# Kernel tuning notes

Measured on AMD Instinct MI355X. Metric: run time of the kernel, lower is better.

Reference implementation:

```python
import jax, jax.numpy as jnp
import numpy as np
from jax import lax

B, T, I, H = 64, 512, 512, 512


def setup_inputs() -> dict:
    key = jax.random.key(0)
    ks = jax.random.split(key, 9)
    s_in = 1.0 / np.sqrt(I)
    s_h = 1.0 / np.sqrt(H)
    return {
        "x": jax.random.normal(ks[0], (B, T, I), dtype=jnp.float32),
        "h0_f": jnp.zeros((B, H), dtype=jnp.float32),
        "h0_b": jnp.zeros((B, H), dtype=jnp.float32),
        # cell_f params (torch Linear: y = x @ W.T + b)
        "Wxf_w": jax.random.uniform(ks[1], (H, I), jnp.float32, -s_in, s_in),
        "Wxf_b": jax.random.uniform(ks[2], (H,), jnp.float32, -s_in, s_in),
        "Whf_w": jax.random.uniform(ks[3], (H, H), jnp.float32, -s_h, s_h),
        # cell_b params
        "Wxb_w": jax.random.uniform(ks[4], (H, I), jnp.float32, -s_in, s_in),
        "Wxb_b": jax.random.uniform(ks[5], (H,), jnp.float32, -s_in, s_in),
        "Whb_w": jax.random.uniform(ks[6], (H, H), jnp.float32, -s_h, s_h),
    }


def _run_dir(x_tbi, h0, Wx_w, Wx_b, Wh_w, reverse):
    # Precompute input projections as one big GEMM (same math as per-step Linear)
    xproj = jnp.einsum("tbi,hi->tbh", x_tbi, Wx_w) + Wx_b  # (T,B,H)

    def step(h, xp):
        h = jnp.tanh(xp + h @ Wh_w.T)
        return h, h

    hT, hs = lax.scan(step, h0, xproj, reverse=reverse)
    return hT, hs  # hs in natural time order even when reverse=True


def reference(x, h0_f, h0_b, Wxf_w, Wxf_b, Whf_w, Wxb_w, Wxb_b, Whb_w):
    x_tbi = jnp.transpose(x, (1, 0, 2))  # (T,B,I)
    hT_f, hs_f = _run_dir(x_tbi, h0_f, Wxf_w, Wxf_b, Whf_w, reverse=False)
    hT_b, hs_b = _run_dir(x_tbi, h0_b, Wxb_w, Wxb_b, Whb_w, reverse=True)
    y = jnp.concatenate([hs_f, hs_b], axis=-1)  # (T,B,2H)
    y = jnp.transpose(y, (1, 0, 2))  # (B,T,2H)
    return y, hT_f, hT_b
```

## Files before the change

### kernel.cpp

```cpp
#include <hip/hip_runtime.h>

#define T_LEN 512
#define B_SZ  64
#define I_SZ  512
#define H_SZ  512

using half8   = __attribute__((ext_vector_type(8))) _Float16;
using half4   = __attribute__((ext_vector_type(4))) _Float16;
using float4v = __attribute__((ext_vector_type(4))) float;

__device__ __forceinline__ float fast_tanh(float x) {
    float e = __expf(2.0f * x);
    return 1.0f - 2.0f * __builtin_amdgcn_rcpf(e + 1.0f);
}

__global__ __launch_bounds__(256) void xproj_kernel(
    const float* __restrict__ x,
    const float* __restrict__ Wf, const float* __restrict__ bf,
    const float* __restrict__ Wb, const float* __restrict__ bb,
    _Float16* __restrict__ xp)
{
    __shared__ _Float16 Ash[64][72];
    __shared__ _Float16 Bsh[64][72];

    const int bid = blockIdx.x;
    const int dir = bid & 1;
    const int nt  = (bid >> 1) & 7;
    const int t   = bid >> 4;
    const float* __restrict__ W    = dir ? Wb : Wf;
    const float* __restrict__ bias = dir ? bb : bf;
    const int n0 = nt * 64;

    const int tid  = threadIdx.x;
    const int row  = tid >> 2;
    const int part = tid & 3;
    const int wv   = tid >> 6;
    const int lane = tid & 63;
    const int lm   = lane & 15;
    const int lq   = lane >> 4;

    float4v acc[4] = {{0,0,0,0},{0,0,0,0},{0,0,0,0},{0,0,0,0}};

    const float* ap = x + ((size_t)row * T_LEN + t) * I_SZ + part * 16;
    const float* bp = W + ((size_t)(n0 + row)) * I_SZ + part * 16;

    for (int k0 = 0; k0 < I_SZ; k0 += 64) {
        float areg[16], breg[16];
        #pragma unroll
        for (int i = 0; i < 16; i++) { areg[i] = ap[k0 + i]; breg[i] = bp[k0 + i]; }
        __syncthreads();
        #pragma unroll
        for (int i = 0; i < 16; i++) {
            Ash[row][part*16 + i] = (_Float16)areg[i];
            Bsh[row][part*16 + i] = (_Float16)breg[i];
        }
        __syncthreads();
        #pragma unroll
        for (int ks = 0; ks < 2; ks++) {
            half8 afr = *(const half8*)&Ash[16*wv + lm][ks*32 + lq*8];
            #pragma unroll
            for (int ns = 0; ns < 4; ns++) {
                half8 bfr = *(const half8*)&Bsh[ns*16 + lm][ks*32 + lq*8];
                acc[ns] = __builtin_amdgcn_mfma_f32_16x16x32_f16(afr, bfr, acc[ns], 0, 0, 0);
            }
        }
    }

    #pragma unroll
    for (int ns = 0; ns < 4; ns++) {
        const int n = n0 + ns*16 + lm;
        const float bv = bias[n];
        #pragma unroll
        for (int j = 0; j < 4; j++) {
            const int b = 16*wv + lq*4 + j;
            xp[(((size_t)dir*T_LEN + t)*B_SZ + b)*H_SZ + n] = (_Float16)(acc[ns][j] + bv);
        }
    }
}

__global__ __launch_bounds__(512, 2) void rnn_kernel(
    const _Float16* __restrict__ xp,
    const float* __restrict__ Whf, const float* __restrict__ Whb,
    const float* __restrict__ h0f, const float* __restrict__ h0b,
    float* __restrict__ out)
{
    const int blk  = blockIdx.x;
    const int dir  = blk >> 2;
    const int b0   = (blk & 3) * 16;
    const int tid  = threadIdx.x;
    const int wv   = tid >> 6;
    const int lane = tid & 63;
    const int lq   = lane >> 4;
    const int lm   = lane & 15;

    const float* __restrict__ Wh = dir ? Whb : Whf;
    const float* __restrict__ h0 = dir ? h0b : h0f;

    __shared__ _Float16 hl[8192];
    __shared__ _Float16 wl[8][16][64][8];

    half8 bw[4][12];
    {
        const float* wr0 = Wh + ((size_t)(wv*64 + lm*4)) * H_SZ + lq*8;
        #pragma unroll
        for (int nt = 0; nt < 4; nt++) {
            const float* wr = wr0 + (size_t)nt * H_SZ;
            #pragma unroll
            for (int kt = 0; kt < 16; kt++) {
                float4v lo = *(const float4v*)(wr + kt*32);
                float4v hi = *(const float4v*)(wr + kt*32 + 4);
                half8 v;
                #pragma unroll
                for (int e = 0; e < 4; e++) { v[e] = (_Float16)lo[e]; v[e+4] = (_Float16)hi[e]; }
                if (kt < 12) bw[nt][kt] = v;
                else *(half8*)&wl[wv][nt*4 + (kt - 12)][lane][0] = v;
            }
        }
    }

    #pragma unroll
    for (int r = 0; r < 2; r++) {
        const int gi  = r*512 + tid;
        const int khi = gi >> 4;
        const int b   = gi & 15;
        const float* p = h0 + (size_t)(b0 + b)*H_SZ + khi*8;
        half8 v;
        #pragma unroll
        for (int e = 0; e < 8; e++) v[e] = (_Float16)p[e];
        *(half8*)&hl[(khi*16 + (b ^ (khi & 15))) * 8] = v;
    }
    __syncthreads();

    const _Float16* wlp = &wl[wv][0][lane][0];

    const int ts = dir ? -1 : 1;
    const int t0 = dir ? (T_LEN - 1) : 0;
    const _Float16* xpt = xp + (((size_t)dir*T_LEN + t0)*B_SZ + (b0 + lq*4))*H_SZ
                             + wv*64 + lm*4;
    const ptrdiff_t xstep = (ptrdiff_t)ts * (B_SZ * H_SZ);
    float* yb = out + ((size_t)(b0 + lq*4)*T_LEN + t0)*1024 + dir*512 + wv*64 + lm*4;
    const ptrdiff_t ystep = (ptrdiff_t)ts * 1024;

    const int khiw = wv*8 + (lm >> 1);
    const int gofs = (lm & 1) * 4;

    half4 xq[4];
    #pragma unroll
    for (int j = 0; j < 4; j++) xq[j] = *(const half4*)(xpt + j*H_SZ);

    #pragma unroll 1
    for (int s = 0; s < T_LEN; s++) {
        float4v acc[4];
        #pragma unroll
        for (int nt = 0; nt < 4; nt++)
            #pragma unroll
            for (int j = 0; j < 4; j++)
                acc[nt][j] = (float)xq[j][nt];

        if (s + 1 < T_LEN) {
            xpt += xstep;
            #pragma unroll
            for (int j = 0; j < 4; j++) xq[j] = *(const half4*)(xpt + j*H_SZ);
        }

        #pragma unroll
        for (int g = 0; g < 3; g++) {
            half8 af[4];
            #pragma unroll
            for (int i = 0; i < 4; i++) {
                const int c = (g*4 + i)*4 + lq;
                af[i] = *(const half8*)&hl[(c*16 + (lm ^ (c & 15))) * 8];
            }
            #pragma unroll
            for (int i = 0; i < 4; i++)
                #pragma unroll
                for (int nt = 0; nt < 4; nt++)
                    acc[nt] = __builtin_amdgcn_mfma_f32_16x16x32_f16(af[i], bw[nt][g*4 + i], acc[nt], 0, 0, 0);
        }
        {
            half8 af[4];
            #pragma unroll
            for (int i = 0; i < 4; i++) {
                const int c = (12 + i)*4 + lq;
                af[i] = *(const half8*)&hl[(c*16 + (lm ^ (c & 15))) * 8];
            }
            #pragma unroll
            for (int i = 0; i < 4; i++)
                #pragma unroll
                for (int nt = 0; nt < 4; nt++) {
                    half8 w = *(const half8*)(wlp + (nt*4 + i)*512);
                    acc[nt] = __builtin_amdgcn_mfma_f32_16x16x32_f16(af[i], w, acc[nt], 0, 0, 0);
                }
        }

        half4 pks[4];
        #pragma unroll
        for (int j = 0; j < 4; j++) {
            float4v v;
            #pragma unroll
            for (int nt = 0; nt < 4; nt++) v[nt] = fast_tanh(acc[nt][j]);
            __builtin_nontemporal_store(v, (float4v*)(yb + (size_t)j*(T_LEN*1024)));
            if (s == T_LEN - 1) {
                float* hp = out + 33554432 + (size_t)dir*32768
                          + (size_t)(b0 + lq*4 + j)*H_SZ + wv*64 + lm*4;
                __builtin_nontemporal_store(v, (float4v*)hp);
            }
            half4 pk;
            #pragma unroll
            for (int nt = 0; nt < 4; nt++) pk[nt] = (_Float16)v[nt];
            pks[j] = pk;
        }
        yb += ystep;

        asm volatile("s_waitcnt lgkmcnt(0)" ::: "memory");
        __builtin_amdgcn_s_barrier();

        #pragma unroll
        for (int j = 0; j < 4; j++)
            *(half4*)&hl[(khiw*16 + ((lq*4 + j) ^ (khiw & 15))) * 8 + gofs] = pks[j];

        asm volatile("s_waitcnt lgkmcnt(0)" ::: "memory");
        __builtin_amdgcn_s_barrier();
    }
}

extern "C" void kernel_launch(void* const* d_in, const int* in_sizes, int n_in,
                              void* d_out, int out_size, void* d_ws, size_t ws_size,
                              hipStream_t stream) {
    const float* x   = (const float*)d_in[0];
    const float* h0f = (const float*)d_in[1];
    const float* h0b = (const float*)d_in[2];
    const float* Wxf = (const float*)d_in[3];
    const float* bxf = (const float*)d_in[4];
    const float* Whf = (const float*)d_in[5];
    const float* Wxb = (const float*)d_in[6];
    const float* bxb = (const float*)d_in[7];
    const float* Whb = (const float*)d_in[8];
    float* out = (float*)d_out;

    _Float16* xpb = (_Float16*)d_ws;

    hipLaunchKernelGGL(xproj_kernel, dim3(8192), dim3(256), 0, stream,
                       x, Wxf, bxf, Wxb, bxb, xpb);
    hipLaunchKernelGGL(rnn_kernel, dim3(8), dim3(512), 0, stream,
                       xpb, Whf, Whb, h0f, h0b, out);
}
```

Before: 1.748 ms.

## Retile input-projection GEMM to 128x128 blocks with swizzled LDS and block order

The input-projection kernel now works on 128x128 output tiles with 2x2 waves each computing 4x4 MFMA tiles. Before, each block covered 64x64 for a single timestep. It loads rows of the flattened (B*T) x matrix contiguously with float4 loads, stores to XOR-swizzled LDS, and remaps block IDs so blocks sharing data run close together. This raises arithmetic intensity and cuts redundant global reads of x and W. The trade-offs are more register pressure and scattered fp16 stores, since output rows map to (t,b) with stride. The recurrent kernel, which likely dominates total time, is unchanged.

New measurement: 1.695 ms. 1.03x faster.

```diff
diff --git a/kernel.cpp b/kernel.cpp
--- a/kernel.cpp
+++ b/kernel.cpp
@@ -20,60 +20,108 @@
     const float* __restrict__ Wb, const float* __restrict__ bb,
     _Float16* __restrict__ xp)
 {
-    __shared__ _Float16 Ash[64][72];
-    __shared__ _Float16 Bsh[64][72];
+    __shared__ _Float16 Ash[8192];
+    __shared__ _Float16 Bsh[8192];
 
     const int bid = blockIdx.x;
-    const int dir = bid & 1;
-    const int nt  = (bid >> 1) & 7;
-    const int t   = bid >> 4;
+    const int swz = (bid & 7) * 256 + (bid >> 3);
+    const int dir = swz & 1;
+    const int nb  = (swz >> 1) & 3;
+    const int mb  = swz >> 3;
+    const int m0  = mb * 128;
+    const int n0  = nb * 128;
+
     const float* __restrict__ W    = dir ? Wb : Wf;
     const float* __restrict__ bias = dir ? bb : bf;
-    const int n0 = nt * 64;
 
     const int tid  = threadIdx.x;
-    const int row  = tid >> 2;
-    const int part = tid & 3;
     const int wv   = tid >> 6;
     const int lane = tid & 63;
     const int lm   = lane & 15;
     const int lq   = lane >> 4;
-
-    float4v acc[4] = {{0,0,0,0},{0,0,0,0},{0,0,0,0},{0,0,0,0}};
-
-    const float* ap = x + ((size_t)row * T_LEN + t) * I_SZ + part * 16;
-    const float* bp = W + ((size_t)(n0 + row)) * I_SZ + part * 16;
+    const int wm   = wv >> 1;
+    const int wn   = wv & 1;
+
+    int rowA[4], ldsA[4];
+    #pragma unroll
+    for (int r = 0; r < 4; r++) {
+        const int q   = r*256 + tid;
+        const int row = q >> 3;
+        const int khi = q & 7;
+        rowA[r] = row;
+        ldsA[r] = (row >> 4)*1024 + (khi*16 + ((row & 15) ^ khi))*8;
+    }
+
+    float4v acc[4][4];
+    #pragma unroll
+    for (int mt = 0; mt < 4; mt++)
+        #pragma unroll
+        for (int nt = 0; nt < 4; nt++)
+            acc[mt][nt] = (float4v){0,0,0,0};
 
     for (int k0 = 0; k0 < I_SZ; k0 += 64) {
-        float areg[16], breg[16];
-        #pragma unroll
-        for (int i = 0; i < 16; i++) { areg[i] = ap[k0 + i]; breg[i] = bp[k0 + i]; }
+        float4v st[16];
+        #pragma unroll
+        for (int r = 0; r < 4; r++) {
+            const int q   = r*256 + tid;
+            const int khi = q & 7;
+            const float* ga = x + (size_t)(m0 + rowA[r])*I_SZ + k0 + khi*8;
+            const float* gb = W + (size_t)(n0 + rowA[r])*I_SZ + k0 + khi*8;
+            st[r*2]     = *(const float4v*)ga;
+            st[r*2 + 1] = *(const float4v*)(ga + 4);
+            st[8 + r*2]     = *(const float4v*)gb;
+            st[8 + r*2 + 1] = *(const float4v*)(gb + 4);
+        }
         __syncthreads();
         #pragma unroll
-        for (int i = 0; i < 16; i++) {
-            Ash[row][part*16 + i] = (_Float16)areg[i];
-            Bsh[row][part*16 + i] = (_Float16)breg[i];
+        for (int r = 0; r < 4; r++) {
+            half8 va, vb;
+            #pragma unroll
+            for (int e = 0; e < 4; e++) {
+                va[e]   = (_Float16)st[r*2][e];
+                va[e+4] = (_Float16)st[r*2+1][e];
+                vb[e]   = (_Float16)st[8+r*2][e];
+                vb[e+4] = (_Float16)st[8+r*2+1][e];
+            }
+            *(half8*)&Ash[ldsA[r]] = va;
+            *(half8*)&Bsh[ldsA[r]] = vb;
         }
         __syncthreads();
+
         #pragma unroll
         for (int ks = 0; ks < 2; ks++) {
-            half8 afr = *(const half8*)&Ash[16*wv + lm][ks*32 + lq*8];
-            #pragma unroll
-            for (int ns = 0; ns < 4; ns++) {
-                half8 bfr = *(const half8*)&Bsh[ns*16 + lm][ks*32 + lq*8];
-                acc[ns] = __builtin_amdgcn_mfma_f32_16x16x32_f16(afr, bfr, acc[ns], 0, 0, 0);
-            }
-        }
-    }
-
-    #pragma unroll
-    for (int ns = 0; ns < 4; ns++) {
-        const int n = n0 + ns*16 + lm;
+            const int khi = ks*4 + lq;
+            const int go  = (khi*16 + (lm ^ khi))*8;
+            half8 afr[4], bfr[4];
+            #pragma unroll
+            for (int mt = 0; mt < 4; mt++)
+                afr[mt] = *(const half8*)&Ash[(wm*4 + mt)*1024 + go];
+            #pragma unroll
+            for (int nt = 0; nt < 4; nt++)
+                bfr[nt] = *(const half8*)&Bsh[(wn*4 + nt)*1024 + go];
+            #pragma unroll
+            for (int mt = 0; mt < 4; mt++)
+                #pragma unroll
+                for (int nt = 0; nt < 4; nt++)
+                    acc[mt][nt] = __builtin_amdgcn_mfma_f32_16x16x32_f16(
+                        afr[mt], bfr[nt], acc[mt][nt], 0, 0, 0);
+        }
+    }
+
+    #pragma unroll
+    for (int nt = 0; nt < 4; nt++) {
+        const int n  = n0 + wn*64 + nt*16 + lm;
         const float bv = bias[n];
         #pragma unroll
-        for (int j = 0; j < 4; j++) {
-            const int b = 16*wv + lq*4 + j;
-            xp[(((size_t)dir*T_LEN + t)*B_SZ + b)*H_SZ + n] = (_Float16)(acc[ns][j] + bv);
+        for (int mt = 0; mt < 4; mt++) {
+            #pragma unroll
+            for (int j = 0; j < 4; j++) {
+                const int m = m0 + wm*64 + mt*16 + lq*4 + j;
+                const int b = m >> 9;
+                const int t = m & 511;
+                xp[(((size_t)dir*T_LEN + t)*B_SZ + b)*H_SZ + n] =
+                    (_Float16)(acc[mt][nt][j] + bv);
+            }
         }
     }
 }
@@ -240,7 +288,7 @@
 
     _Float16* xpb = (_Float16*)d_ws;
 
-    hipLaunchKernelGGL(xproj_kernel, dim3(8192), dim3(256), 0, stream,
+    hipLaunchKernelGGL(xproj_kernel, dim3(2048), dim3(256), 0, stream,
                        x, Wxf, bxf, Wxb, bxb, xpb);
     hipLaunchKernelGGL(rnn_kernel, dim3(8), dim3(512), 0, stream,
                        xpb, Whf, Whb, h0f, h0b, out);
```
